# Optimization experiments

Measured on AMD Instinct MI355X. Metric: run time of the kernel, lower is better.

## Reference

```python
import jax, jax.numpy as jnp
import numpy as np
from jax import lax

KERNEL = 2  # kernel_size, forced by the (s3-1, s4-1, s5-1) output reshape


def setup_inputs() -> dict:
    key = jax.random.key(0)
    kx, kw = jax.random.split(key)
    x = jax.random.normal(kx, (4, 16, 32, 32, 32), dtype=jnp.float32)
    w = jax.random.normal(kw, (512, 128), dtype=jnp.float32)  # (d1, d2=C*2^3)
    return {"x": x, "w": w}


def _gaussian_kernel(x, w):
    N, C, D, H, W = x.shape
    d1, d2 = w.shape
    # 3D unfold with kernel 2, stride 1, no padding -> (N, C*8, D-1, H-1, W-1)
    patches = lax.conv_general_dilated_patches(
        x,
        filter_shape=(KERNEL, KERNEL, KERNEL),
        window_strides=(1, 1, 1),
        padding='VALID',
    )
    P = (D - 1) * (H - 1) * (W - 1)
    y = patches.reshape(N, d2, P).transpose(0, 2, 1)  # (N, P, d2)
    # sum((y - w)^2) expanded as ||y||^2 - 2 y.w + ||w||^2 to avoid the
    # (N, P, d1, d2) broadcasted difference tensor.
    y_sq = jnp.sum(y * y, axis=-1, keepdims=True)           # (N, P, 1)
    w_sq = jnp.sum(w * w, axis=-1)                          # (d1,)
    cross = jnp.einsum('npd,kd->npk', y, w)                 # (N, P, d1)
    dist = y_sq - 2.0 * cross + w_sq                        # (N, P, d1)
    out = jnp.exp(-dist)
    return out.transpose(0, 2, 1).reshape(N, d1, D - 1, H - 1, W - 1)


def reference(x, w):
    return _gaussian_kernel(x, w)
```

## Files before the change

### kernel.cpp

```cpp
#include <hip/hip_runtime.h>

typedef unsigned char u8;
typedef float f32x4 __attribute__((ext_vector_type(4)));

#define P_OUT 29791
#define NCH   512

__device__ __forceinline__ unsigned pk4_fp8(float a, float b, float c, float d) {
  int v = __builtin_amdgcn_cvt_pk_fp8_f32(a, b, 0, false);
  v = __builtin_amdgcn_cvt_pk_fp8_f32(c, d, v, true);
  return (unsigned)v;
}

__global__ void wprep_kernel(const float* __restrict__ w,
                             u8* __restrict__ wb, float* __restrict__ wsq) {
  const int tid = threadIdx.x;
  const int g = blockIdx.x * 16 + (tid >> 4);
  const int c = tid & 15;
  const float4* wr = (const float4*)(w + g * 128 + c * 8);
  float4 f0 = wr[0], f1 = wr[1];
  float s = f0.x*f0.x + f0.y*f0.y + f0.z*f0.z + f0.w*f0.w
          + f1.x*f1.x + f1.y*f1.y + f1.z*f1.z + f1.w*f1.w;
#pragma unroll
  for (int m = 1; m < 16; m <<= 1) s += __shfl_xor(s, m, 64);
  uint2 pk;
  pk.x = pk4_fp8(f0.x, f0.y, f0.z, f0.w);
  pk.y = pk4_fp8(f1.x, f1.y, f1.z, f1.w);
  *(uint2*)(wb + g * 128 + c * 8) = pk;
  if (c == 0) wsq[g] = s;
}

#define GLDS(g, l) __builtin_amdgcn_global_load_lds(                         \
    (const __attribute__((address_space(1))) unsigned int*)(g),              \
    (__attribute__((address_space(3))) unsigned int*)(l), 16, 0, 0)

__global__ __launch_bounds__(512)
void gauss_fused_kernel(const float* __restrict__ x,
                        const u8* __restrict__ wb,
                        const float* __restrict__ wsq,
                        float* __restrict__ out) {
  __shared__ __align__(16) u8 Ws[128 * 128];
  __shared__ __align__(16) float Xs[9216];

  const int bid = blockIdx.x;
  const int tile = (bid & 7) * 248 + (bid >> 3);
  const unsigned pq = (unsigned)tile & 3u;
  const unsigned t2 = (unsigned)tile >> 2;
  const unsigned d  = t2 % 31u;
  const unsigned t3 = t2 / 31u;
  const unsigned ct = t3 & 3u;
  const unsigned nb = t3 >> 2;

  const int h0 = pq * 8;
  const int nrows = (pq < 3) ? 248 : 217;
  const int tp0 = d * 961 + pq * 248;
  const int c0 = ct * 128;

  const int tid = threadIdx.x;
  const int wid = tid >> 6;
  const int lane = tid & 63;
  const int quad = lane >> 4;
  const int col = lane & 15;
  const int wch = wid & 1;
  const int wp = wid >> 1;

#pragma unroll
  for (int t = 0; t < 2; ++t) {
    const int Lb = (wid * 2 + t) * 64;
    const int L = Lb + lane;
    const int row = L >> 3;
    const int jc = (L & 7) ^ (row & 7);
    GLDS(wb + (size_t)(c0 + row) * 128 + jc * 16, &Ws[Lb * 16]);
  }

#pragma unroll
  for (int t = 0; t < 5; ++t) {
    if (t < 4 || wid < 4) {
      const int Lb = t * 512 + wid * 64;
      const int L = Lb + lane;
      const int row = L >> 3;
      const int jc = L & 7;
      const unsigned c = (unsigned)row / 18u;
      const unsigned rr = (unsigned)row - c * 18u;
      const unsigned kd = rr / 9u;
      const unsigned hq = rr - kd * 9u;
      const int hg = h0 + (int)hq;
      const int hcl = (hg < 31) ? hg : 31;
      GLDS(x + (((size_t)(nb * 16 + c)) << 15) + (d + kd) * 1024 + hcl * 32 + jc * 4,
           &Xs[Lb * 4]);
    }
  }

  int rb[4];
  int xoff[4];
#pragma unroll
  for (int j = 0; j < 4; ++j) {
    rb[j] = wp * 64 + j * 16 + col;
    const unsigned rc = (unsigned)((rb[j] < nrows) ? rb[j] : (nrows - 1));
    const unsigned hh = rc / 31u;
    const unsigned wv = rc - hh * 31u;
    xoff[j] = (int)(hh * 32 + wv);
  }

  __syncthreads();

  long long B[4][4];
  float sq[4] = {0.f, 0.f, 0.f, 0.f};
#pragma unroll
  for (int ks = 0; ks < 4; ++ks) {
    const int cc = ks * 4 + quad;
    const float* xb = &Xs[cc * 576];
#pragma unroll
    for (int j = 0; j < 4; ++j) {
      const float* pB = xb + xoff[j];
      const float v0 = pB[0],   v1 = pB[1],   v2 = pB[32],  v3 = pB[33];
      const float v4 = pB[288], v5 = pB[289], v6 = pB[320], v7 = pB[321];
      sq[j] += v0*v0 + v1*v1 + v2*v2 + v3*v3 + v4*v4 + v5*v5 + v6*v6 + v7*v7;
      const unsigned lo = pk4_fp8(v0, v1, v2, v3);
      const unsigned hi = pk4_fp8(v4, v5, v6, v7);
      B[ks][j] = (long long)(((unsigned long long)hi << 32) | lo);
    }
  }
#pragma unroll
  for (int j = 0; j < 4; ++j) {
    sq[j] += __shfl_xor(sq[j], 16, 64);
    sq[j] += __shfl_xor(sq[j], 32, 64);
  }

  f32x4 acc[4][4];
#pragma unroll
  for (int i = 0; i < 4; ++i)
#pragma unroll
    for (int j = 0; j < 4; ++j) acc[i][j] = (f32x4){0.f, 0.f, 0.f, 0.f};

  const int c16b = quad >> 1;
  const int hoff = (quad & 1) * 8;
#pragma unroll
  for (int ks = 0; ks < 4; ++ks) {
    long long a[4];
#pragma unroll
    for (int i = 0; i < 4; ++i) {
      const int rowA = wch * 64 + i * 16 + col;
      const int pa = (ks * 2 + c16b) ^ (rowA & 7);
      a[i] = *(const long long*)&Ws[rowA * 128 + pa * 16 + hoff];
    }
#pragma unroll
    for (int i = 0; i < 4; ++i)
#pragma unroll
      for (int j = 0; j < 4; ++j)
        acc[i][j] = __builtin_amdgcn_mfma_f32_16x16x32_fp8_fp8(a[i], B[ks][j],
                                                               acc[i][j], 0, 0, 0);
  }

#pragma unroll
  for (int i = 0; i < 4; ++i) {
#pragma unroll
    for (int r = 0; r < 4; ++r) {
      const int ch = c0 + wch * 64 + i * 16 + quad * 4 + r;
      const float wsv = wsq[ch];
      float* ob = out + ((size_t)(nb * NCH + ch)) * P_OUT;
#pragma unroll
      for (int j = 0; j < 4; ++j)
        if (rb[j] < nrows)
          ob[tp0 + rb[j]] = __expf(2.f * acc[i][j][r] - sq[j] - wsv);
    }
  }
}

extern "C" void kernel_launch(void* const* d_in, const int* in_sizes, int n_in,
                              void* d_out, int out_size, void* d_ws, size_t ws_size,
                              hipStream_t stream) {
  const float* x = (const float*)d_in[0];
  const float* w = (const float*)d_in[1];
  float* out = (float*)d_out;
  char* ws = (char*)d_ws;
  u8* wb     = (u8*)ws;
  float* wsq = (float*)(ws + 65536);

  wprep_kernel<<<32, 256, 0, stream>>>(w, wb, wsq);
  gauss_fused_kernel<<<1984, 512, 0, stream>>>(x, wb, wsq, out);
}
```

Measured before the change: 298.0 us.

## Loop each block over four h-slabs with W reuse and prefetched X

The fused kernel now runs 256-thread blocks, two per CU, and launches half as many. Each block keeps its 128-channel W tile in LDS and walks four 4-row h-slabs in a loop. Once the current slab's fp8 B fragments are in registers, the next slab of x is loaded into a smaller shared buffer, so that load overlaps the MFMA and exp/store work. This cuts repeated W loads and block launch overhead, at the cost of extra barriers per iteration and fewer waves per block.

Measured after the change: 274.8 us. 7.8% less time.

```diff
diff --git a/kernel.cpp b/kernel.cpp
--- a/kernel.cpp
+++ b/kernel.cpp
@@ -34,26 +34,22 @@
     (const __attribute__((address_space(1))) unsigned int*)(g),              \
     (__attribute__((address_space(3))) unsigned int*)(l), 16, 0, 0)
 
-__global__ __launch_bounds__(512)
+__global__ __launch_bounds__(256, 2)
 void gauss_fused_kernel(const float* __restrict__ x,
                         const u8* __restrict__ wb,
                         const float* __restrict__ wsq,
                         float* __restrict__ out) {
   __shared__ __align__(16) u8 Ws[128 * 128];
-  __shared__ __align__(16) float Xs[9216];
+  __shared__ __align__(16) float Xs[5120];
 
   const int bid = blockIdx.x;
-  const int tile = (bid & 7) * 248 + (bid >> 3);
-  const unsigned pq = (unsigned)tile & 3u;
-  const unsigned t2 = (unsigned)tile >> 2;
+  const int tile = (bid & 7) * 124 + (bid >> 3);
+  const unsigned hh = (unsigned)tile & 1u;
+  const unsigned t2 = (unsigned)tile >> 1;
   const unsigned d  = t2 % 31u;
   const unsigned t3 = t2 / 31u;
   const unsigned ct = t3 & 3u;
   const unsigned nb = t3 >> 2;
-
-  const int h0 = pq * 8;
-  const int nrows = (pq < 3) ? 248 : 217;
-  const int tp0 = d * 961 + pq * 248;
   const int c0 = ct * 128;
 
   const int tid = threadIdx.x;
@@ -65,25 +61,26 @@
   const int wp = wid >> 1;
 
 #pragma unroll
-  for (int t = 0; t < 2; ++t) {
-    const int Lb = (wid * 2 + t) * 64;
+  for (int t = 0; t < 4; ++t) {
+    const int Lb = (wid * 4 + t) * 64;
     const int L = Lb + lane;
     const int row = L >> 3;
     const int jc = (L & 7) ^ (row & 7);
     GLDS(wb + (size_t)(c0 + row) * 128 + jc * 16, &Ws[Lb * 16]);
   }
 
-#pragma unroll
-  for (int t = 0; t < 5; ++t) {
-    if (t < 4 || wid < 4) {
-      const int Lb = t * 512 + wid * 64;
+  {
+    const int h0 = (int)hh * 16;
+#pragma unroll
+    for (int t = 0; t < 5; ++t) {
+      const int Lb = t * 256 + wid * 64;
       const int L = Lb + lane;
       const int row = L >> 3;
       const int jc = L & 7;
-      const unsigned c = (unsigned)row / 18u;
-      const unsigned rr = (unsigned)row - c * 18u;
-      const unsigned kd = rr / 9u;
-      const unsigned hq = rr - kd * 9u;
+      const unsigned c = (unsigned)row / 10u;
+      const unsigned rr = (unsigned)row - c * 10u;
+      const unsigned kd = rr / 5u;
+      const unsigned hq = rr - kd * 5u;
       const int hg = h0 + (int)hq;
       const int hcl = (hg < 31) ? hg : 31;
       GLDS(x + (((size_t)(nb * 16 + c)) << 15) + (d + kd) * 1024 + hcl * 32 + jc * 4,
@@ -91,79 +88,109 @@
     }
   }
 
-  int rb[4];
-  int xoff[4];
-#pragma unroll
-  for (int j = 0; j < 4; ++j) {
-    rb[j] = wp * 64 + j * 16 + col;
-    const unsigned rc = (unsigned)((rb[j] < nrows) ? rb[j] : (nrows - 1));
-    const unsigned hh = rc / 31u;
-    const unsigned wv = rc - hh * 31u;
-    xoff[j] = (int)(hh * 32 + wv);
-  }
-
-  __syncthreads();
-
-  long long B[4][4];
-  float sq[4] = {0.f, 0.f, 0.f, 0.f};
-#pragma unroll
-  for (int ks = 0; ks < 4; ++ks) {
-    const int cc = ks * 4 + quad;
-    const float* xb = &Xs[cc * 576];
-#pragma unroll
-    for (int j = 0; j < 4; ++j) {
-      const float* pB = xb + xoff[j];
-      const float v0 = pB[0],   v1 = pB[1],   v2 = pB[32],  v3 = pB[33];
-      const float v4 = pB[288], v5 = pB[289], v6 = pB[320], v7 = pB[321];
-      sq[j] += v0*v0 + v1*v1 + v2*v2 + v3*v3 + v4*v4 + v5*v5 + v6*v6 + v7*v7;
-      const unsigned lo = pk4_fp8(v0, v1, v2, v3);
-      const unsigned hi = pk4_fp8(v4, v5, v6, v7);
-      B[ks][j] = (long long)(((unsigned long long)hi << 32) | lo);
-    }
-  }
-#pragma unroll
-  for (int j = 0; j < 4; ++j) {
-    sq[j] += __shfl_xor(sq[j], 16, 64);
-    sq[j] += __shfl_xor(sq[j], 32, 64);
-  }
-
-  f32x4 acc[4][4];
-#pragma unroll
-  for (int i = 0; i < 4; ++i)
-#pragma unroll
-    for (int j = 0; j < 4; ++j) acc[i][j] = (f32x4){0.f, 0.f, 0.f, 0.f};
-
   const int c16b = quad >> 1;
   const int hoff = (quad & 1) * 8;
-#pragma unroll
-  for (int ks = 0; ks < 4; ++ks) {
-    long long a[4];
+
+  __syncthreads();
+
+  for (int it = 0; it < 4; ++it) {
+    const int h0 = (int)hh * 16 + it * 4;
+    const int nrows = (hh == 1 && it == 3) ? 93 : 124;
+    const int tp0 = (int)d * 961 + h0 * 31;
+
+    int rb[4];
+    int xoff[4];
+#pragma unroll
+    for (int j = 0; j < 4; ++j) {
+      rb[j] = wp * 64 + j * 16 + col;
+      const unsigned rc = (unsigned)((rb[j] < nrows) ? rb[j] : (nrows - 1));
+      const unsigned hl = rc / 31u;
+      const unsigned wv = rc - hl * 31u;
+      xoff[j] = (int)(hl * 32 + wv);
+    }
+
+    long long B[4][4];
+    float sq[4] = {0.f, 0.f, 0.f, 0.f};
+#pragma unroll
+    for (int ks = 0; ks < 4; ++ks) {
+      const int cc = ks * 4 + quad;
+      const float* xb = &Xs[cc * 320];
+#pragma unroll
+      for (int j = 0; j < 4; ++j) {
+        const float* pB = xb + xoff[j];
+        const float v0 = pB[0],   v1 = pB[1],   v2 = pB[32],  v3 = pB[33];
+        const float v4 = pB[160], v5 = pB[161], v6 = pB[192], v7 = pB[193];
+        sq[j] += v0*v0 + v1*v1 + v2*v2 + v3*v3 + v4*v4 + v5*v5 + v6*v6 + v7*v7;
+        const unsigned lo = pk4_fp8(v0, v1, v2, v3);
+        const unsigned hi = pk4_fp8(v4, v5, v6, v7);
+        B[ks][j] = (long long)(((unsigned long long)hi << 32) | lo);
+      }
+    }
+#pragma unroll
+    for (int j = 0; j < 4; ++j) {
+      sq[j] += __shfl_xor(sq[j], 16, 64);
+      sq[j] += __shfl_xor(sq[j], 32, 64);
+    }
+
+    __syncthreads();
+
+    if (it < 3) {
+      const int hn = h0 + 4;
+#pragma unroll
+      for (int t = 0; t < 5; ++t) {
+        const int Lb = t * 256 + wid * 64;
+        const int L = Lb + lane;
+        const int row = L >> 3;
+        const int jc = L & 7;
+        const unsigned c = (unsigned)row / 10u;
+        const unsigned rr = (unsigned)row - c * 10u;
+        const unsigned kd = rr / 5u;
+        const unsigned hq = rr - kd * 5u;
+        const int hg = hn + (int)hq;
+        const int hcl = (hg < 31) ? hg : 31;
+        GLDS(x + (((size_t)(nb * 16 + c)) << 15) + (d + kd) * 1024 + hcl * 32 + jc * 4,
+             &Xs[Lb * 4]);
+      }
+    }
+
+    f32x4 acc[4][4];
+#pragma unroll
+    for (int i = 0; i < 4; ++i)
+#pragma unroll
+      for (int j = 0; j < 4; ++j) acc[i][j] = (f32x4){0.f, 0.f, 0.f, 0.f};
+
+#pragma unroll
+    for (int ks = 0; ks < 4; ++ks) {
+      long long a[4];
+#pragma unroll
+      for (int i = 0; i < 4; ++i) {
+        const int rowA = wch * 64 + i * 16 + col;
+        const int pa = (ks * 2 + c16b) ^ (rowA & 7);
+        a[i] = *(const long long*)&Ws[rowA * 128 + pa * 16 + hoff];
+      }
+#pragma unroll
+      for (int i = 0; i < 4; ++i)
+#pragma unroll
+        for (int j = 0; j < 4; ++j)
+          acc[i][j] = __builtin_amdgcn_mfma_f32_16x16x32_fp8_fp8(a[i], B[ks][j],
+                                                                 acc[i][j], 0, 0, 0);
+    }
+
 #pragma unroll
     for (int i = 0; i < 4; ++i) {
-      const int rowA = wch * 64 + i * 16 + col;
-      const int pa = (ks * 2 + c16b) ^ (rowA & 7);
-      a[i] = *(const long long*)&Ws[rowA * 128 + pa * 16 + hoff];
-    }
-#pragma unroll
-    for (int i = 0; i < 4; ++i)
-#pragma unroll
-      for (int j = 0; j < 4; ++j)
-        acc[i][j] = __builtin_amdgcn_mfma_f32_16x16x32_fp8_fp8(a[i], B[ks][j],
-                                                               acc[i][j], 0, 0, 0);
-  }
-
-#pragma unroll
-  for (int i = 0; i < 4; ++i) {
-#pragma unroll
-    for (int r = 0; r < 4; ++r) {
-      const int ch = c0 + wch * 64 + i * 16 + quad * 4 + r;
-      const float wsv = wsq[ch];
-      float* ob = out + ((size_t)(nb * NCH + ch)) * P_OUT;
-#pragma unroll
-      for (int j = 0; j < 4; ++j)
-        if (rb[j] < nrows)
-          ob[tp0 + rb[j]] = __expf(2.f * acc[i][j][r] - sq[j] - wsv);
-    }
+#pragma unroll
+      for (int r = 0; r < 4; ++r) {
+        const int ch = c0 + wch * 64 + i * 16 + quad * 4 + r;
+        const float wsv = wsq[ch];
+        float* ob = out + ((size_t)(nb * NCH + ch)) * P_OUT;
+#pragma unroll
+        for (int j = 0; j < 4; ++j)
+          if (rb[j] < nrows)
+            ob[tp0 + rb[j]] = __expf(2.f * acc[i][j][r] - sq[j] - wsv);
+      }
+    }
+
+    if (it < 3) __syncthreads();
   }
 }
 
@@ -178,5 +205,5 @@
   float* wsq = (float*)(ws + 65536);
 
   wprep_kernel<<<32, 256, 0, stream>>>(w, wb, wsq);
-  gauss_fused_kernel<<<1984, 512, 0, stream>>>(x, wb, wsq, out);
-}
+  gauss_fused_kernel<<<992, 256, 0, stream>>>(x, wb, wsq, out);
+}
```
